# Optimization experiments

Measured on AMD Instinct MI355X. Metric: run time of the kernel, lower is better.

Reference implementation:

```python
import jax, jax.numpy as jnp
import numpy as np

N_HEAD = 8


def setup_inputs() -> dict:
    key = jax.random.key(0)
    ks = jax.random.split(key, 5)
    D = 512
    q = jax.random.normal(ks[0], (2, 4096, D), dtype=jnp.float32)
    s = 0.02  # init scale for weights
    Wq = jax.random.normal(ks[1], (D, D), dtype=jnp.float32) * s
    Wk = jax.random.normal(ks[2], (D, D), dtype=jnp.float32) * s
    Wv = jax.random.normal(ks[3], (D, D), dtype=jnp.float32) * s
    Wo = jax.random.normal(ks[4], (D, D), dtype=jnp.float32) * s
    z = jnp.zeros((D,), dtype=jnp.float32)
    return {"q": q, "Wq": Wq, "bq": z, "Wk": Wk, "bk": z, "Wv": Wv, "bv": z, "Wo": Wo, "bo": z}


def _split_heads(x, n_head):
    # (b, s, c) -> (b, h, s, c//h)
    b, s, c = x.shape
    return x.reshape(b, s, n_head, c // n_head).transpose(0, 2, 1, 3)


def reference(q, Wq, bq, Wk, bk, Wv, bv, Wo, bo):
    # Linear projections (nn.Linear: x @ W.T + b); self-attention (kv = q)
    qp = _split_heads(q @ Wq.T + bq, N_HEAD)  # (b, h, s, dh)
    kp = _split_heads(q @ Wk.T + bk, N_HEAD)
    vp = _split_heads(q @ Wv.T + bv, N_HEAD)
    dh = qp.shape[-1]
    scale = 1.0 / jnp.sqrt(jnp.asarray(dh, dtype=qp.dtype))
    # unfused MATH-backend SDPA: full [b,h,s,s] scores, stable softmax, no dropout (eval)
    scores = jnp.einsum("bhqd,bhkd->bhqk", qp, kp) * scale
    probs = jax.nn.softmax(scores, axis=-1)
    attn = jnp.einsum("bhqk,bhkd->bhqd", probs, vp)  # (b, h, s, dh)
    # merge heads: (b, h, s, dh) -> (b, s, h*dh)
    b, h, s, _ = attn.shape
    merged = attn.transpose(0, 2, 1, 3).reshape(b, s, h * dh)
    return merged @ Wo.T + bo
```

## Files before the change

kernel.cpp:

```cpp
#include <hip/hip_runtime.h>
#include <hip/hip_bf16.h>
#include <math.h>

typedef __attribute__((ext_vector_type(8))) short bf16x8;
typedef __attribute__((ext_vector_type(4))) float f32x4;
typedef __attribute__((ext_vector_type(16))) float f32x16;

__device__ __forceinline__ unsigned short f2bf(float f) {
    union { float f; unsigned int u; } v; v.f = f;
    unsigned int u = v.u;
    u += 0x7fffu + ((u >> 16) & 1u);
    return (unsigned short)(u >> 16);
}

__device__ __forceinline__ f32x16 mfma32(bf16x8 a, bf16x8 b, f32x16 c) {
    return __builtin_amdgcn_mfma_f32_32x32x16_bf16(a, b, c, 0, 0, 0);
}

__device__ __forceinline__ unsigned packbf2(float a, float b) {
    __hip_bfloat162 h = __float22bfloat162_rn(float2{a, b});
    union { __hip_bfloat162 h; unsigned u; } v; v.h = h;
    return v.u;
}

__device__ __forceinline__ void pl32swap(unsigned &a, unsigned &b) {
    asm volatile("v_permlane32_swap_b32 %0, %1" : "+v"(a), "+v"(b));
}

template<int A_BF16>
__device__ __forceinline__ void gemm_body(const void* Ap, const float* W,
                                          f32x4 (&acc)[4][4],
                                          unsigned short (*As)[40], unsigned short (*Bs)[40],
                                          int bm, int bn, int t)
{
    constexpr int Kdim = 512;
    const int lane = t & 63, g = lane >> 4, c = lane & 15;
    const int w = t >> 6, wr = w >> 1, wc = w & 1;

    uint4  paB[2];
    float4 paF[4];
    float4 pw[4];
    const int ccB = (t & 3) * 8, r0B = t >> 2;
    const int c4  = (t & 7) * 4, r0F = t >> 3;

    if (A_BF16) {
        const unsigned short* A = (const unsigned short*)Ap;
        for (int p = 0; p < 2; ++p)
            paB[p] = *(const uint4*)(A + (size_t)(bm + r0B + p * 64) * Kdim + ccB);
    } else {
        const float* A = (const float*)Ap;
        for (int p = 0; p < 4; ++p)
            paF[p] = *(const float4*)(A + (size_t)(bm + r0F + p * 32) * Kdim + c4);
    }
    for (int p = 0; p < 4; ++p)
        pw[p] = *(const float4*)(W + (size_t)(bn + r0F + p * 32) * Kdim + c4);

    for (int k0 = 0; k0 < Kdim; k0 += 32) {
        __syncthreads();
        if (A_BF16) {
            for (int p = 0; p < 2; ++p)
                *(uint4*)&As[r0B + p * 64][ccB] = paB[p];
        } else {
            for (int p = 0; p < 4; ++p) {
                float4 v = paF[p];
                ushort4 hv;
                hv.x = f2bf(v.x); hv.y = f2bf(v.y); hv.z = f2bf(v.z); hv.w = f2bf(v.w);
                *(ushort4*)&As[r0F + p * 32][c4] = hv;
            }
        }
        for (int p = 0; p < 4; ++p) {
            float4 v = pw[p];
            ushort4 hv;
            hv.x = f2bf(v.x); hv.y = f2bf(v.y); hv.z = f2bf(v.z); hv.w = f2bf(v.w);
            *(ushort4*)&Bs[r0F + p * 32][c4] = hv;
        }
        __syncthreads();
        if (k0 + 32 < Kdim) {
            const int kn = k0 + 32;
            if (A_BF16) {
                const unsigned short* A = (const unsigned short*)Ap;
                for (int p = 0; p < 2; ++p)
                    paB[p] = *(const uint4*)(A + (size_t)(bm + r0B + p * 64) * Kdim + kn + ccB);
            } else {
                const float* A = (const float*)Ap;
                for (int p = 0; p < 4; ++p)
                    paF[p] = *(const float4*)(A + (size_t)(bm + r0F + p * 32) * Kdim + kn + c4);
            }
            for (int p = 0; p < 4; ++p)
                pw[p] = *(const float4*)(W + (size_t)(bn + r0F + p * 32) * Kdim + kn + c4);
        }
        bf16x8 af[4], bfr[4];
        for (int i = 0; i < 4; ++i)
            af[i] = *(const bf16x8*)&As[wr * 64 + i * 16 + c][g * 8];
        for (int j = 0; j < 4; ++j)
            bfr[j] = *(const bf16x8*)&Bs[wc * 64 + j * 16 + c][g * 8];
        for (int i = 0; i < 4; ++i)
            for (int j = 0; j < 4; ++j)
                acc[i][j] = __builtin_amdgcn_mfma_f32_16x16x32_bf16(af[i], bfr[j], acc[i][j], 0, 0, 0);
    }
}

__global__ __launch_bounds__(256, 2)
void gemm_qkv(const float* __restrict__ q,
              const float* __restrict__ Wq, const float* __restrict__ bq,
              const float* __restrict__ Wk, const float* __restrict__ bk,
              const float* __restrict__ Wv, const float* __restrict__ bv,
              unsigned short* __restrict__ Qo, unsigned short* __restrict__ Ko,
              unsigned short* __restrict__ Vo)
{
    __shared__ unsigned short As[128][40];
    __shared__ unsigned short Bs[128][40];
    const int t = threadIdx.x, z = blockIdx.z;
    const int lane = t & 63, g = lane >> 4, c = lane & 15;
    const int w = t >> 6, wr = w >> 1, wc = w & 1;
    const int bm = blockIdx.x * 128, bn = blockIdx.y * 128;

    const float* W    = (z == 0) ? Wq : (z == 1) ? Wk : Wv;
    const float* bias = (z == 0) ? bq : (z == 1) ? bk : bv;
    unsigned short* Out = (z == 0) ? Qo : (z == 1) ? Ko : Vo;
    const float osc = (z == 0) ? 0.125f * 1.44269504f : 1.0f;

    f32x4 acc[4][4] = {};
    gemm_body<0>((const void*)q, W, acc, As, Bs, bm, bn, t);

    float bv4[4];
    for (int j = 0; j < 4; ++j) bv4[j] = bias[bn + wc * 64 + j * 16 + c];
    for (int i = 0; i < 4; ++i)
        for (int j = 0; j < 4; ++j)
            for (int r = 0; r < 4; ++r) {
                int m = bm + wr * 64 + i * 16 + 4 * g + r;
                int n = bn + wc * 64 + j * 16 + c;
                float val = (acc[i][j][r] + bv4[j]) * osc;
                int b = m >> 12, s = m & 4095, h = n >> 6, d = n & 63;
                if (z < 2)
                    Out[((((size_t)b * 8 + h) * 4096 + s) << 6) + d] = f2bf(val);
                else
                    Out[(((size_t)b * 8 + h) * 64 + d) * 4096 + s] = f2bf(val);
            }
}

__global__ __launch_bounds__(256, 2)
void gemm_out(const unsigned short* __restrict__ A, const float* __restrict__ W,
              const float* __restrict__ bias, float* __restrict__ Out)
{
    __shared__ unsigned short As[128][40];
    __shared__ unsigned short Bs[128][40];
    const int t = threadIdx.x;
    const int lane = t & 63, g = lane >> 4, c = lane & 15;
    const int w = t >> 6, wr = w >> 1, wc = w & 1;
    const int bm = blockIdx.x * 128, bn = blockIdx.y * 128;

    f32x4 acc[4][4] = {};
    gemm_body<1>((const void*)A, W, acc, As, Bs, bm, bn, t);

    float bv4[4];
    for (int j = 0; j < 4; ++j) bv4[j] = bias[bn + wc * 64 + j * 16 + c];
    for (int i = 0; i < 4; ++i)
        for (int j = 0; j < 4; ++j)
            for (int r = 0; r < 4; ++r) {
                int m = bm + wr * 64 + i * 16 + 4 * g + r;
                int n = bn + wc * 64 + j * 16 + c;
                Out[(size_t)m * 512 + n] = acc[i][j][r] + bv4[j];
            }
}

__global__ __launch_bounds__(512, 2)
void attn256(const unsigned short* __restrict__ Q, const unsigned short* __restrict__ Kh,
             const unsigned short* __restrict__ VT, unsigned short* __restrict__ Mo)
{
    __shared__ unsigned short Ks[2 * 128 * 64];
    __shared__ unsigned short Vs[2 * 64 * 128];

    const int t = threadIdx.x, w = t >> 6, l = t & 63;
    const int l5 = l >> 5, c31 = l & 31;
    const int idp = (blockIdx.x & 7) * 32 + (blockIdx.x >> 3);
    const int bh = idp >> 4;
    const int q0 = (idp & 15) * 256;
    const unsigned short* Qb = Q + (size_t)bh * 4096 * 64;
    const unsigned short* Kb = Kh + (size_t)bh * 4096 * 64;
    const unsigned short* Vb = VT + (size_t)bh * 64 * 4096;

    const int qr = q0 + w * 32 + c31;
    bf16x8 qv0 = *(const bf16x8*)(Qb + (size_t)qr * 64 + 8 * l5);
    bf16x8 qv1 = *(const bf16x8*)(Qb + (size_t)qr * 64 + 16 + 8 * l5);
    bf16x8 qv2 = *(const bf16x8*)(Qb + (size_t)qr * 64 + 32 + 8 * l5);
    bf16x8 qv3 = *(const bf16x8*)(Qb + (size_t)qr * 64 + 48 + 8 * l5);

    f32x16 o0 = {}, o1 = {}, lac = {};
    const f32x16 zro = {};

    bf16x8 ones;
    #pragma unroll
    for (int i = 0; i < 8; ++i) ones[i] = (short)0x3F80;

    const int sl01 = (l5 ^ (l & 1)) * 8;
    const int ka0 = c31 * 64 + (0 ^ (l & 6)) * 8 + sl01;
    const int ka1 = c31 * 64 + (2 ^ (l & 6)) * 8 + sl01;
    const int ka2 = c31 * 64 + (4 ^ (l & 6)) * 8 + sl01;
    const int ka3 = c31 * 64 + (6 ^ (l & 6)) * 8 + sl01;
    const int va0 = c31 * 128 + (0 ^ (l & 6)) * 8 + sl01;
    const int va1 = c31 * 128 + (2 ^ (l & 6)) * 8 + sl01;
    const int va2 = c31 * 128 + (4 ^ (l & 6)) * 8 + sl01;
    const int va3 = c31 * 128 + (6 ^ (l & 6)) * 8 + sl01;

    const int srow = t >> 3, s0 = t & 7;
    const int scol = s0 * 8, r7 = srow & 7;
    const int woffK  = srow * 64 + ((s0 ^ r7) << 3);
    const int woffKB = (64 + srow) * 64 + ((s0 ^ r7) << 3);
    const int woffV  = srow * 128 + ((s0 ^ r7) << 3);
    const int woffVB = srow * 128 + ((8 + (s0 ^ r7)) << 3);
    const unsigned short* kpA = Kb + (size_t)srow * 64 + scol;
    const unsigned short* vpA = Vb + (size_t)srow * 4096 + scol;

    uint4 kaA = *(const uint4*)(kpA);
    uint4 kaB = *(const uint4*)(kpA + 64 * 64);
    uint4 vaA = *(const uint4*)(vpA);
    uint4 vaB = *(const uint4*)(vpA + 64);
    *(uint4*)&Ks[woffK]  = kaA;
    *(uint4*)&Ks[woffKB] = kaB;
    *(uint4*)&Vs[woffV]  = vaA;
    *(uint4*)&Vs[woffVB] = vaB;

    auto half_iter = [&](int kbase, int vbase) {
        f32x16 ta, tb;
        __builtin_amdgcn_s_setprio(1);
        ta = mfma32(*(const bf16x8*)&Ks[kbase + ka0], qv0, zro);
        ta = mfma32(*(const bf16x8*)&Ks[kbase + ka1], qv1, ta);
        ta = mfma32(*(const bf16x8*)&Ks[kbase + ka2], qv2, ta);
        ta = mfma32(*(const bf16x8*)&Ks[kbase + ka3], qv3, ta);
        tb = mfma32(*(const bf16x8*)&Ks[kbase + 2048 + ka0], qv0, zro);
        tb = mfma32(*(const bf16x8*)&Ks[kbase + 2048 + ka1], qv1, tb);
        tb = mfma32(*(const bf16x8*)&Ks[kbase + 2048 + ka2], qv2, tb);
        tb = mfma32(*(const bf16x8*)&Ks[kbase + 2048 + ka3], qv3, tb);
        __builtin_amdgcn_s_setprio(0);

        union { unsigned u[4]; bf16x8 v; } p0, p1, p2, p3;
        {
            unsigned x0 = packbf2(exp2f(ta[0]),  exp2f(ta[1]));
            unsigned x1 = packbf2(exp2f(ta[2]),  exp2f(ta[3]));
            unsigned y0 = packbf2(exp2f(ta[4]),  exp2f(ta[5]));
            unsigned y1 = packbf2(exp2f(ta[6]),  exp2f(ta[7]));
            pl32swap(x0, y0); pl32swap(x1, y1);
            p0.u[0] = x0; p0.u[1] = x1; p0.u[2] = y0; p0.u[3] = y1;
            x0 = packbf2(exp2f(ta[8]),  exp2f(ta[9]));
            x1 = packbf2(exp2f(ta[10]), exp2f(ta[11]));
            y0 = packbf2(exp2f(ta[12]), exp2f(ta[13]));
            y1 = packbf2(exp2f(ta[14]), exp2f(ta[15]));
            pl32swap(x0, y0); pl32swap(x1, y1);
            p1.u[0] = x0; p1.u[1] = x1; p1.u[2] = y0; p1.u[3] = y1;
            x0 = packbf2(exp2f(tb[0]),  exp2f(tb[1]));
            x1 = packbf2(exp2f(tb[2]),  exp2f(tb[3]));
            y0 = packbf2(exp2f(tb[4]),  exp2f(tb[5]));
            y1 = packbf2(exp2f(tb[6]),  exp2f(tb[7]));
            pl32swap(x0, y0); pl32swap(x1, y1);
            p2.u[0] = x0; p2.u[1] = x1; p2.u[2] = y0; p2.u[3] = y1;
            x0 = packbf2(exp2f(tb[8]),  exp2f(tb[9]));
            x1 = packbf2(exp2f(tb[10]), exp2f(tb[11]));
            y0 = packbf2(exp2f(tb[12]), exp2f(tb[13]));
            y1 = packbf2(exp2f(tb[14]), exp2f(tb[15]));
            pl32swap(x0, y0); pl32swap(x1, y1);
            p3.u[0] = x0; p3.u[1] = x1; p3.u[2] = y0; p3.u[3] = y1;
        }

        __builtin_amdgcn_s_setprio(1);
        o0  = mfma32(p0.v, *(const bf16x8*)&Vs[vbase + va0], o0);
        o1  = mfma32(p0.v, *(const bf16x8*)&Vs[vbase + 4096 + va0], o1);
        lac = mfma32(p0.v, ones, lac);
        o0  = mfma32(p1.v, *(const bf16x8*)&Vs[vbase + va1], o0);
        o1  = mfma32(p1.v, *(const bf16x8*)&Vs[vbase + 4096 + va1], o1);
        lac = mfma32(p1.v, ones, lac);
        o0  = mfma32(p2.v, *(const bf16x8*)&Vs[vbase + va2], o0);
        o1  = mfma32(p2.v, *(const bf16x8*)&Vs[vbase + 4096 + va2], o1);
        lac = mfma32(p2.v, ones, lac);
        o0  = mfma32(p3.v, *(const bf16x8*)&Vs[vbase + va3], o0);
        o1  = mfma32(p3.v, *(const bf16x8*)&Vs[vbase + 4096 + va3], o1);
        lac = mfma32(p3.v, ones, lac);
        __builtin_amdgcn_s_setprio(0);
    };

    auto tile_iter = [&](int it, int kb, int vb) {
        __syncthreads();
        if (it < 31) {
            const unsigned short* kp = kpA + (size_t)(it + 1) * 8192;
            const unsigned short* vp = vpA + (it + 1) * 128;
            kaA = *(const uint4*)(kp);
            kaB = *(const uint4*)(kp + 64 * 64);
            vaA = *(const uint4*)(vp);
            vaB = *(const uint4*)(vp + 64);
        }
        half_iter(kb, vb);
        half_iter(kb + 4096, vb + 64);
        if (it < 31) {
            int ko = kb ^ 8192, vo = vb ^ 8192;
            *(uint4*)&Ks[ko + woffK]  = kaA;
            *(uint4*)&Ks[ko + woffKB] = kaB;
            *(uint4*)&Vs[vo + woffV]  = vaA;
            *(uint4*)&Vs[vo + woffVB] = vaB;
        }
    };

    for (int it2 = 0; it2 < 32; it2 += 2) {
        tile_iter(it2, 0, 0);
        tile_iter(it2 + 1, 8192, 8192);
    }

    const int b = bh >> 3, h = bh & 7;
    #pragma unroll
    for (int i = 0; i < 16; ++i) {
        int qrow = (i & 3) + 8 * (i >> 2) + 4 * l5;
        float inv = 1.f / lac[i];
        size_t m = (size_t)(b * 4096 + q0 + w * 32 + qrow) * 512 + h * 64 + c31;
        Mo[m]      = f2bf(o0[i] * inv);
        Mo[m + 32] = f2bf(o1[i] * inv);
    }
}

extern "C" void kernel_launch(void* const* d_in, const int* in_sizes, int n_in,
                              void* d_out, int out_size, void* d_ws, size_t ws_size,
                              hipStream_t stream) {
    const float* q  = (const float*)d_in[0];
    const float* Wq = (const float*)d_in[1];
    const float* bq = (const float*)d_in[2];
    const float* Wk = (const float*)d_in[3];
    const float* bk = (const float*)d_in[4];
    const float* Wv = (const float*)d_in[5];
    const float* bv = (const float*)d_in[6];
    const float* Wo = (const float*)d_in[7];
    const float* bo = (const float*)d_in[8];

    unsigned short* Qb = (unsigned short*)d_ws;
    unsigned short* Kb = Qb + (size_t)16 * 4096 * 64;
    unsigned short* Vt = Kb + (size_t)16 * 4096 * 64;
    unsigned short* Mg = Vt + (size_t)16 * 4096 * 64;

    dim3 gb(256);
    dim3 gqkv(64, 4, 3);
    gemm_qkv<<<gqkv, gb, 0, stream>>>(q, Wq, bq, Wk, bk, Wv, bv, Qb, Kb, Vt);

    attn256<<<dim3(256), dim3(512), 0, stream>>>(Qb, Kb, Vt, Mg);

    dim3 gg(64, 4);
    gemm_out<<<gg, gb, 0, stream>>>(Mg, Wo, bo, (float*)d_out);
}
```

Before: 165.1 us.

## Triple-buffer K/V shared tiles with two-ahead register prefetch in attention

Replaces the double-buffered K/V LDS staging with a three-slot ring. Global loads are now issued two tiles ahead into alternating register sets, and the LDS write for the next tile happens at the start of each iteration. The aim is to hide global-load latency behind more compute. In exchange, LDS use per block rises by half, which may reduce occupancy at two blocks per CU, and register pressure grows from holding a second set of prefetch registers.

```diff
diff --git a/kernel.cpp b/kernel.cpp
--- a/kernel.cpp
+++ b/kernel.cpp
@@ -168,8 +168,8 @@
 void attn256(const unsigned short* __restrict__ Q, const unsigned short* __restrict__ Kh,
              const unsigned short* __restrict__ VT, unsigned short* __restrict__ Mo)
 {
-    __shared__ unsigned short Ks[2 * 128 * 64];
-    __shared__ unsigned short Vs[2 * 64 * 128];
+    __shared__ unsigned short Ks[3 * 128 * 64];
+    __shared__ unsigned short Vs[3 * 64 * 128];
 
     const int t = threadIdx.x, w = t >> 6, l = t & 63;
     const int l5 = l >> 5, c31 = l & 31;
@@ -212,14 +212,19 @@
     const unsigned short* kpA = Kb + (size_t)srow * 64 + scol;
     const unsigned short* vpA = Vb + (size_t)srow * 4096 + scol;
 
-    uint4 kaA = *(const uint4*)(kpA);
-    uint4 kaB = *(const uint4*)(kpA + 64 * 64);
-    uint4 vaA = *(const uint4*)(vpA);
-    uint4 vaB = *(const uint4*)(vpA + 64);
-    *(uint4*)&Ks[woffK]  = kaA;
-    *(uint4*)&Ks[woffKB] = kaB;
-    *(uint4*)&Vs[woffV]  = vaA;
-    *(uint4*)&Vs[woffVB] = vaB;
+    uint4 kA0 = *(const uint4*)(kpA);
+    uint4 kA1 = *(const uint4*)(kpA + 4096);
+    uint4 vA0 = *(const uint4*)(vpA);
+    uint4 vA1 = *(const uint4*)(vpA + 64);
+    *(uint4*)&Ks[woffK]  = kA0;
+    *(uint4*)&Ks[woffKB] = kA1;
+    *(uint4*)&Vs[woffV]  = vA0;
+    *(uint4*)&Vs[woffVB] = vA1;
+    kA0 = *(const uint4*)(kpA + 8192);
+    kA1 = *(const uint4*)(kpA + 8192 + 4096);
+    vA0 = *(const uint4*)(vpA + 128);
+    vA1 = *(const uint4*)(vpA + 128 + 64);
+    uint4 kB0, kB1, vB0, vB1;
 
     auto half_iter = [&](int kbase, int vbase) {
         f32x16 ta, tb;
@@ -278,30 +283,54 @@
         __builtin_amdgcn_s_setprio(0);
     };
 
-    auto tile_iter = [&](int it, int kb, int vb) {
-        __syncthreads();
-        if (it < 31) {
-            const unsigned short* kp = kpA + (size_t)(it + 1) * 8192;
-            const unsigned short* vp = vpA + (it + 1) * 128;
-            kaA = *(const uint4*)(kp);
-            kaB = *(const uint4*)(kp + 64 * 64);
-            vaA = *(const uint4*)(vp);
-            vaB = *(const uint4*)(vp + 64);
-        }
-        half_iter(kb, vb);
-        half_iter(kb + 4096, vb + 64);
-        if (it < 31) {
-            int ko = kb ^ 8192, vo = vb ^ 8192;
-            *(uint4*)&Ks[ko + woffK]  = kaA;
-            *(uint4*)&Ks[ko + woffKB] = kaB;
-            *(uint4*)&Vs[vo + woffV]  = vaA;
-            *(uint4*)&Vs[vo + woffVB] = vaB;
-        }
-    };
-
+    int cur = 0;
     for (int it2 = 0; it2 < 32; it2 += 2) {
-        tile_iter(it2, 0, 0);
-        tile_iter(it2 + 1, 8192, 8192);
+        {
+            const int it = it2;
+            __syncthreads();
+            const int nxt = (cur == 2) ? 0 : cur + 1;
+            const int bn_ = nxt * 8192;
+            *(uint4*)&Ks[bn_ + woffK]  = kA0;
+            *(uint4*)&Ks[bn_ + woffKB] = kA1;
+            *(uint4*)&Vs[bn_ + woffV]  = vA0;
+            *(uint4*)&Vs[bn_ + woffVB] = vA1;
+            if (it <= 29) {
+                const unsigned short* kp = kpA + (size_t)(it + 2) * 8192;
+                const unsigned short* vp = vpA + (it + 2) * 128;
+                kB0 = *(const uint4*)(kp);
+                kB1 = *(const uint4*)(kp + 4096);
+                vB0 = *(const uint4*)(vp);
+                vB1 = *(const uint4*)(vp + 64);
+            }
+            const int bc = cur * 8192;
+            half_iter(bc, bc);
+            half_iter(bc + 4096, bc + 64);
+            cur = nxt;
+        }
+        {
+            const int it = it2 + 1;
+            __syncthreads();
+            const int nxt = (cur == 2) ? 0 : cur + 1;
+            if (it <= 30) {
+                const int bn_ = nxt * 8192;
+                *(uint4*)&Ks[bn_ + woffK]  = kB0;
+                *(uint4*)&Ks[bn_ + woffKB] = kB1;
+                *(uint4*)&Vs[bn_ + woffV]  = vB0;
+                *(uint4*)&Vs[bn_ + woffVB] = vB1;
+            }
+            if (it <= 29) {
+                const unsigned short* kp = kpA + (size_t)(it + 2) * 8192;
+                const unsigned short* vp = vpA + (it + 2) * 128;
+                kA0 = *(const uint4*)(kp);
+                kA1 = *(const uint4*)(kp + 4096);
+                vA0 = *(const uint4*)(vp);
+                vA1 = *(const uint4*)(vp + 64);
+            }
+            const int bc = cur * 8192;
+            half_iter(bc, bc);
+            half_iter(bc + 4096, bc + 64);
+            cur = nxt;
+        }
     }
 
     const int b = bh >> 3, h = bh & 7;
```

Result: no change. 166.7 us (+0.9%).

## Double KV tile to 256 keys per barrier and unify K/V LDS layout

Applied to the files above, without the earlier changes.

The attention kernel now stages 256 keys of K and V per pipeline step instead of 128, halving the number of barriers and outer iterations. Each step issues eight global loads per thread instead of four. V is stored in LDS as 64-wide sub-tiles, so the V read offsets reuse the K swizzle pattern. Shared memory doubles to 64 KB per block and launch bounds drop to one block per CU, giving up a second resident block and adding register pressure from the extra prefetch registers.

```diff
diff --git a/kernel.cpp b/kernel.cpp
--- a/kernel.cpp
+++ b/kernel.cpp
@@ -164,12 +164,12 @@
             }
 }
 
-__global__ __launch_bounds__(512, 2)
+__global__ __launch_bounds__(512, 1)
 void attn256(const unsigned short* __restrict__ Q, const unsigned short* __restrict__ Kh,
              const unsigned short* __restrict__ VT, unsigned short* __restrict__ Mo)
 {
-    __shared__ unsigned short Ks[2 * 128 * 64];
-    __shared__ unsigned short Vs[2 * 64 * 128];
+    __shared__ unsigned short Ks[2 * 4 * 64 * 64];
+    __shared__ unsigned short Vs[2 * 4 * 64 * 64];
 
     const int t = threadIdx.x, w = t >> 6, l = t & 63;
     const int l5 = l >> 5, c31 = l & 31;
@@ -198,40 +198,41 @@
     const int ka1 = c31 * 64 + (2 ^ (l & 6)) * 8 + sl01;
     const int ka2 = c31 * 64 + (4 ^ (l & 6)) * 8 + sl01;
     const int ka3 = c31 * 64 + (6 ^ (l & 6)) * 8 + sl01;
-    const int va0 = c31 * 128 + (0 ^ (l & 6)) * 8 + sl01;
-    const int va1 = c31 * 128 + (2 ^ (l & 6)) * 8 + sl01;
-    const int va2 = c31 * 128 + (4 ^ (l & 6)) * 8 + sl01;
-    const int va3 = c31 * 128 + (6 ^ (l & 6)) * 8 + sl01;
 
     const int srow = t >> 3, s0 = t & 7;
-    const int scol = s0 * 8, r7 = srow & 7;
-    const int woffK  = srow * 64 + ((s0 ^ r7) << 3);
-    const int woffKB = (64 + srow) * 64 + ((s0 ^ r7) << 3);
-    const int woffV  = srow * 128 + ((s0 ^ r7) << 3);
-    const int woffVB = srow * 128 + ((8 + (s0 ^ r7)) << 3);
+    const int scol = s0 * 8;
+    const int woffK = srow * 64 + ((s0 ^ (srow & 7)) << 3);
     const unsigned short* kpA = Kb + (size_t)srow * 64 + scol;
     const unsigned short* vpA = Vb + (size_t)srow * 4096 + scol;
 
-    uint4 kaA = *(const uint4*)(kpA);
-    uint4 kaB = *(const uint4*)(kpA + 64 * 64);
-    uint4 vaA = *(const uint4*)(vpA);
-    uint4 vaB = *(const uint4*)(vpA + 64);
-    *(uint4*)&Ks[woffK]  = kaA;
-    *(uint4*)&Ks[woffKB] = kaB;
-    *(uint4*)&Vs[woffV]  = vaA;
-    *(uint4*)&Vs[woffVB] = vaB;
-
-    auto half_iter = [&](int kbase, int vbase) {
+    uint4 pk0 = *(const uint4*)(kpA);
+    uint4 pk1 = *(const uint4*)(kpA + 4096);
+    uint4 pk2 = *(const uint4*)(kpA + 8192);
+    uint4 pk3 = *(const uint4*)(kpA + 12288);
+    uint4 pv0 = *(const uint4*)(vpA);
+    uint4 pv1 = *(const uint4*)(vpA + 64);
+    uint4 pv2 = *(const uint4*)(vpA + 128);
+    uint4 pv3 = *(const uint4*)(vpA + 192);
+    *(uint4*)&Ks[woffK]          = pk0;
+    *(uint4*)&Ks[4096  + woffK]  = pk1;
+    *(uint4*)&Ks[8192  + woffK]  = pk2;
+    *(uint4*)&Ks[12288 + woffK]  = pk3;
+    *(uint4*)&Vs[woffK]          = pv0;
+    *(uint4*)&Vs[4096  + woffK]  = pv1;
+    *(uint4*)&Vs[8192  + woffK]  = pv2;
+    *(uint4*)&Vs[12288 + woffK]  = pv3;
+
+    auto quarter_iter = [&](int qb) {
         f32x16 ta, tb;
         __builtin_amdgcn_s_setprio(1);
-        ta = mfma32(*(const bf16x8*)&Ks[kbase + ka0], qv0, zro);
-        ta = mfma32(*(const bf16x8*)&Ks[kbase + ka1], qv1, ta);
-        ta = mfma32(*(const bf16x8*)&Ks[kbase + ka2], qv2, ta);
-        ta = mfma32(*(const bf16x8*)&Ks[kbase + ka3], qv3, ta);
-        tb = mfma32(*(const bf16x8*)&Ks[kbase + 2048 + ka0], qv0, zro);
-        tb = mfma32(*(const bf16x8*)&Ks[kbase + 2048 + ka1], qv1, tb);
-        tb = mfma32(*(const bf16x8*)&Ks[kbase + 2048 + ka2], qv2, tb);
-        tb = mfma32(*(const bf16x8*)&Ks[kbase + 2048 + ka3], qv3, tb);
+        ta = mfma32(*(const bf16x8*)&Ks[qb + ka0], qv0, zro);
+        ta = mfma32(*(const bf16x8*)&Ks[qb + ka1], qv1, ta);
+        ta = mfma32(*(const bf16x8*)&Ks[qb + ka2], qv2, ta);
+        ta = mfma32(*(const bf16x8*)&Ks[qb + ka3], qv3, ta);
+        tb = mfma32(*(const bf16x8*)&Ks[qb + 2048 + ka0], qv0, zro);
+        tb = mfma32(*(const bf16x8*)&Ks[qb + 2048 + ka1], qv1, tb);
+        tb = mfma32(*(const bf16x8*)&Ks[qb + 2048 + ka2], qv2, tb);
+        tb = mfma32(*(const bf16x8*)&Ks[qb + 2048 + ka3], qv3, tb);
         __builtin_amdgcn_s_setprio(0);
 
         union { unsigned u[4]; bf16x8 v; } p0, p1, p2, p3;
@@ -263,45 +264,55 @@
         }
 
         __builtin_amdgcn_s_setprio(1);
-        o0  = mfma32(p0.v, *(const bf16x8*)&Vs[vbase + va0], o0);
-        o1  = mfma32(p0.v, *(const bf16x8*)&Vs[vbase + 4096 + va0], o1);
+        o0  = mfma32(p0.v, *(const bf16x8*)&Vs[qb + ka0], o0);
+        o1  = mfma32(p0.v, *(const bf16x8*)&Vs[qb + 2048 + ka0], o1);
         lac = mfma32(p0.v, ones, lac);
-        o0  = mfma32(p1.v, *(const bf16x8*)&Vs[vbase + va1], o0);
-        o1  = mfma32(p1.v, *(const bf16x8*)&Vs[vbase + 4096 + va1], o1);
+        o0  = mfma32(p1.v, *(const bf16x8*)&Vs[qb + ka1], o0);
+        o1  = mfma32(p1.v, *(const bf16x8*)&Vs[qb + 2048 + ka1], o1);
         lac = mfma32(p1.v, ones, lac);
-        o0  = mfma32(p2.v, *(const bf16x8*)&Vs[vbase + va2], o0);
-        o1  = mfma32(p2.v, *(const bf16x8*)&Vs[vbase + 4096 + va2], o1);
+        o0  = mfma32(p2.v, *(const bf16x8*)&Vs[qb + ka2], o0);
+        o1  = mfma32(p2.v, *(const bf16x8*)&Vs[qb + 2048 + ka2], o1);
         lac = mfma32(p2.v, ones, lac);
-        o0  = mfma32(p3.v, *(const bf16x8*)&Vs[vbase + va3], o0);
-        o1  = mfma32(p3.v, *(const bf16x8*)&Vs[vbase + 4096 + va3], o1);
+        o0  = mfma32(p3.v, *(const bf16x8*)&Vs[qb + ka3], o0);
+        o1  = mfma32(p3.v, *(const bf16x8*)&Vs[qb + 2048 + ka3], o1);
         lac = mfma32(p3.v, ones, lac);
         __builtin_amdgcn_s_setprio(0);
     };
 
-    auto tile_iter = [&](int it, int kb, int vb) {
+    auto tile_iter = [&](int it, int kb) {
         __syncthreads();
-        if (it < 31) {
-            const unsigned short* kp = kpA + (size_t)(it + 1) * 8192;
-            const unsigned short* vp = vpA + (it + 1) * 128;
-            kaA = *(const uint4*)(kp);
-            kaB = *(const uint4*)(kp + 64 * 64);
-            vaA = *(const uint4*)(vp);
-            vaB = *(const uint4*)(vp + 64);
-        }
-        half_iter(kb, vb);
-        half_iter(kb + 4096, vb + 64);
-        if (it < 31) {
-            int ko = kb ^ 8192, vo = vb ^ 8192;
-            *(uint4*)&Ks[ko + woffK]  = kaA;
-            *(uint4*)&Ks[ko + woffKB] = kaB;
-            *(uint4*)&Vs[vo + woffV]  = vaA;
-            *(uint4*)&Vs[vo + woffVB] = vaB;
+        if (it < 15) {
+            const unsigned short* kp = kpA + (size_t)(it + 1) * 16384;
+            const unsigned short* vp = vpA + (it + 1) * 256;
+            pk0 = *(const uint4*)(kp);
+            pk1 = *(const uint4*)(kp + 4096);
+            pk2 = *(const uint4*)(kp + 8192);
+            pk3 = *(const uint4*)(kp + 12288);
+            pv0 = *(const uint4*)(vp);
+            pv1 = *(const uint4*)(vp + 64);
+            pv2 = *(const uint4*)(vp + 128);
+            pv3 = *(const uint4*)(vp + 192);
+        }
+        quarter_iter(kb);
+        quarter_iter(kb + 4096);
+        quarter_iter(kb + 8192);
+        quarter_iter(kb + 12288);
+        if (it < 15) {
+            int ko = kb ^ 16384;
+            *(uint4*)&Ks[ko + woffK]          = pk0;
+            *(uint4*)&Ks[ko + 4096  + woffK]  = pk1;
+            *(uint4*)&Ks[ko + 8192  + woffK]  = pk2;
+            *(uint4*)&Ks[ko + 12288 + woffK]  = pk3;
+            *(uint4*)&Vs[ko + woffK]          = pv0;
+            *(uint4*)&Vs[ko + 4096  + woffK]  = pv1;
+            *(uint4*)&Vs[ko + 8192  + woffK]  = pv2;
+            *(uint4*)&Vs[ko + 12288 + woffK]  = pv3;
         }
     };
 
-    for (int it2 = 0; it2 < 32; it2 += 2) {
-        tile_iter(it2, 0, 0);
-        tile_iter(it2 + 1, 8192, 8192);
+    for (int it2 = 0; it2 < 16; it2 += 2) {
+        tile_iter(it2, 0);
+        tile_iter(it2 + 1, 16384);
     }
 
     const int b = bh >> 3, h = bh & 7;
```

Measured after the change: 162.6 us. Within noise of the previous version (-1.5%).
